# Performance work log

Hardware: AMD Instinct MI355X
Metric: run time of the kernel (lower is better)

## Reference

```python
import jax, jax.numpy as jnp
import numpy as np
from jax import lax

YXS = [(100, 250), (250, 250), (400, 250)]
HWS = [(50, 400), (50, 400), (50, 400)]
RATIO = 0.8
RCNN_THRES = 0.25
YOLO_THRES = 0.45
NMS_THRES = 0.4


def setup_inputs() -> dict:
    key = jax.random.key(0)
    ks = jax.random.split(key, 6)
    img = jax.random.uniform(ks[0], (1, 3, 500, 500), dtype=jnp.float32)
    patch0 = jax.random.normal(ks[1], (3, 50, 400), dtype=jnp.float32)
    patch1 = jax.random.normal(ks[2], (3, 50, 400), dtype=jnp.float32)
    patch2 = jax.random.normal(ks[3], (3, 50, 400), dtype=jnp.float32)
    rcnn_probs = jax.random.uniform(ks[4], (6144, 81), dtype=jnp.float32)
    boxes = jax.random.uniform(ks[5], (6144, 6), dtype=jnp.float32)
    return {"img": img, "patch0": patch0, "patch1": patch1, "patch2": patch2,
            "rcnn_probs": rcnn_probs, "boxes": boxes}


def _iou_matrix(b):
    # b: [M,4] center format (x, y, w, h) -> pairwise IoU [M,M]
    x1 = b[:, 0] - b[:, 2] * 0.5
    x2 = b[:, 0] + b[:, 2] * 0.5
    y1 = b[:, 1] - b[:, 3] * 0.5
    y2 = b[:, 1] + b[:, 3] * 0.5
    iw = jnp.maximum(jnp.minimum(x2[:, None], x2[None, :]) - jnp.maximum(x1[:, None], x1[None, :]), 0.0)
    ih = jnp.maximum(jnp.minimum(y2[:, None], y2[None, :]) - jnp.maximum(y1[:, None], y1[None, :]), 0.0)
    inter = iw * ih
    area = b[:, 2] * b[:, 3]
    union = area[:, None] + area[None, :] - inter
    return inter / jnp.maximum(union, 1e-12)


def _box_loss(c5, c4, mask):
    # per-box clamp/log loss on cls_conf (c5) and det_conf (c4), masked sum
    s = 1.0 / (0.5 - YOLO_THRES)
    l = (-jnp.clip((c5 - YOLO_THRES) * s, 0.0, 1.0) * jnp.log(1.0 - c5 + 0.01)
         - jnp.clip((c4 - YOLO_THRES) * s, 0.0, 1.0) * jnp.log(1.0 - c4 + 0.01))
    return jnp.sum(jnp.where(mask, l, 0.0))


def reference(img, patch0, patch1, patch2, rcnn_probs, boxes):
    # --- patch blending ---
    for (y, x), (h, w), p in zip(YXS, HWS, (patch0, patch1, patch2)):
        img = img.at[0, :, y - h // 2:y - h // 2 + h, x - w // 2:x - w // 2 + w].add(p)
    # clamp-violation penalty: (-img[img<0]).sum() + (img[img>1]-1).sum()
    p_loss = jnp.sum(jnp.maximum(-img, 0.0)) + jnp.sum(jnp.maximum(img - 1.0, 0.0))
    img = jnp.clip(img, 0.0, 1.0)

    # --- rcnn postprocessing loss ---
    prob = jnp.max(rcnn_probs[:, :-1], axis=-1)
    rmask = prob > RCNN_THRES
    b_prob = rcnn_probs[:, -1]
    r_loss = -jnp.sum(jnp.where(rmask, jnp.log(b_prob + 0.001), 0.0))
    r_loss += -jnp.sum(jnp.where(rmask,
                                 jnp.clip((prob - RCNN_THRES) / (0.3 - RCNN_THRES), 0.0, 1.0)
                                 * jnp.log(1.0 - prob + 0.001), 0.0))

    # --- yolo per-box loss + greedy IoU-NMS loss ---
    conf = boxes[:, 4]
    valid = conf > YOLO_THRES
    b_loss = _box_loss(boxes[:, 5], conf, valid)

    M = boxes.shape[0]
    order = jnp.argsort(-conf)
    sb = boxes[order]          # sorted by det_conf desc
    sv = valid[order]
    iou = _iou_matrix(sb[:, :4])  # [M,M]
    idx = jnp.arange(M)

    def body(keep, i):
        sup = (iou[i] > NMS_THRES) & (idx > i) & keep[i]
        return keep & ~sup, None

    keep, _ = lax.scan(body, sv, idx)
    b_nms_loss = _box_loss(sb[:, 5], sb[:, 4], keep)

    b_cnt = jnp.sum(valid.astype(jnp.float32))
    b_nms_cnt = jnp.maximum(jnp.sum(keep.astype(jnp.float32)), 1.0)
    yolo_loss = b_loss + b_nms_loss * (b_cnt / b_nms_cnt)

    loss = r_loss * RATIO + yolo_loss + p_loss
    return loss
```

## Files before the change

### kernel.cpp

```cpp
#include <hip/hip_runtime.h>
#include <hip/hip_bf16.h>
#include <stdint.h>

#define RCNN_THRES 0.25f
#define YOLO_THRES 0.45f
#define NMS_THRES  0.4f

#define M_BOXES 6144
#define NWORDS  96
#define SORT_N  4096

#define PL_BLOCKS 733
#define RL_BLOCKS 384
#define BL_BLOCKS 6
#define P_ELEMS  750000
#define MB_BLOCKS 1024

typedef unsigned long long u64;

__device__ inline float wave_sum(float v) {
#pragma unroll
    for (int o = 32; o > 0; o >>= 1) v += __shfl_xor(v, o);
    return v;
}
__device__ inline float wave_max(float v) {
#pragma unroll
    for (int o = 32; o > 0; o >>= 1) v = fmaxf(v, __shfl_xor(v, o));
    return v;
}

__device__ inline u64 readlane_u64(u64 v, int l) {
    unsigned lo = (unsigned)__builtin_amdgcn_readlane((int)(unsigned)v, l);
    unsigned hi = (unsigned)__builtin_amdgcn_readlane((int)(unsigned)(v >> 32), l);
    return ((u64)hi << 32) | (u64)lo;
}

__device__ inline float box_loss_term(float c5, float c4) {
    float a = fminf(fmaxf((c5 - YOLO_THRES) * 20.0f, 0.0f), 1.0f);
    float b = fminf(fmaxf((c4 - YOLO_THRES) * 20.0f, 0.0f), 1.0f);
    return -a * logf(1.0f - c5 + 0.01f) - b * logf(1.0f - c4 + 0.01f);
}

__device__ inline bool iou_gt(float x1a, float y1a, float x2a, float y2a, float aa,
                              float x1b, float y1b, float x2b, float y2b, float ab) {
    float iw = fmaxf(fminf(x2a, x2b) - fmaxf(x1a, x1b), 0.0f);
    float ih = fmaxf(fminf(y2a, y2b) - fmaxf(y1a, y1b), 0.0f);
    float inter = iw * ih;
    float uni = aa + ab - inter;
    return (inter / fmaxf(uni, 1e-12f)) > NMS_THRES;
}

__device__ inline u64 vw_word(int w, int nv) {
    int rem = nv - (w << 6);
    if (rem >= 64) return ~0ull;
    if (rem <= 0) return 0ull;
    return (1ull << rem) - 1ull;
}

__global__ __launch_bounds__(1024) void sort_and_losses(
    const float* __restrict__ boxes,
    const float* __restrict__ img, const float* __restrict__ p0,
    const float* __restrict__ p1, const float* __restrict__ p2,
    const float* __restrict__ probs,
    float* __restrict__ sx1, float* __restrict__ sy1,
    float* __restrict__ sx2, float* __restrict__ sy2,
    float* __restrict__ sarea, float* __restrict__ sconf, float* __restrict__ sc5,
    int* __restrict__ nvp, float* __restrict__ acc) {
    const int bid = blockIdx.x;
    const int tid = threadIdx.x, lane = tid & 63, wid = tid >> 6;

    if (bid == 0) {
        __shared__ u64 keys[SORT_N];
        __shared__ u64 bwords[96];
        __shared__ int wcnt[97];
#pragma unroll
        for (int s = 0; s < 6; ++s) {
            int p = tid + s * 1024;
            bool valid = boxes[p * 6 + 4] > YOLO_THRES;
            u64 b = __ballot(valid);
            int chunk = s * 16 + (tid >> 6);
            if (lane == 0) { bwords[chunk] = b; wcnt[chunk] = __popcll(b); }
        }
#pragma unroll
        for (int s = 0; s < 4; ++s) keys[tid + s * 1024] = 0ull;
        __syncthreads();
        if (tid == 0) {
            int run = 0;
            for (int i = 0; i < 96; ++i) { int t = wcnt[i]; wcnt[i] = run; run += t; }
            wcnt[96] = run;
            *nvp = run;
        }
        __syncthreads();
#pragma unroll
        for (int s = 0; s < 6; ++s) {
            int p = tid + s * 1024;
            if (boxes[p * 6 + 4] > YOLO_THRES) {
                int chunk = s * 16 + (tid >> 6);
                u64 b = bwords[chunk];
                int pos = wcnt[chunk] + __popcll(b & ((1ull << lane) - 1ull));
                if (pos < SORT_N) {
                    unsigned int bits = __float_as_uint(boxes[p * 6 + 4]);
                    keys[pos] = ((u64)bits << 13) | (u64)(8191 - p);
                }
            }
        }
        for (int k = 2; k <= SORT_N; k <<= 1) {
            for (int j = k >> 1; j > 0; j >>= 1) {
                __syncthreads();
#pragma unroll
                for (int s = 0; s < SORT_N / 2048; ++s) {
                    int q = tid + s * 1024;
                    int i = ((q & ~(j - 1)) << 1) | (q & (j - 1));
                    int p2 = i | j;
                    u64 a = keys[i], b = keys[p2];
                    bool up = ((i & k) == 0);
                    if ((a < b) == up) { keys[i] = b; keys[p2] = a; }
                }
            }
        }
        __syncthreads();
        const int nv = wcnt[96];
#pragma unroll
        for (int s = 0; s < 4; ++s) {
            int p = tid + s * 1024;
            if (p < nv) {
                int idx = 8191 - (int)(keys[p] & 0x1FFFull);
                const float* b6 = boxes + idx * 6;
                float x = b6[0], y = b6[1], wd = b6[2], ht = b6[3];
                sx1[p] = x - wd * 0.5f;
                sx2[p] = x + wd * 0.5f;
                sy1[p] = y - ht * 0.5f;
                sy2[p] = y + ht * 0.5f;
                sarea[p] = wd * ht;
                sconf[p] = b6[4];
                sc5[p] = b6[5];
            }
        }
        return;
    }

    __shared__ float fred[32];
    if (bid < 1 + PL_BLOCKS) {
        int e = (bid - 1) * 1024 + tid;
        float local = 0.0f;
        if (e < P_ELEMS) {
            float v = img[e];
            int c = e / 250000;
            int rem = e - c * 250000;
            int y = rem / 500;
            int x = rem - y * 500;
            if (x >= 50 && x < 450) {
                int px = x - 50;
                if (y >= 75 && y < 125)       v += p0[c * 20000 + (y - 75) * 400 + px];
                else if (y >= 225 && y < 275) v += p1[c * 20000 + (y - 225) * 400 + px];
                else if (y >= 375 && y < 425) v += p2[c * 20000 + (y - 375) * 400 + px];
            }
            local = fmaxf(-v, 0.0f) + fmaxf(v - 1.0f, 0.0f);
        }
        local = wave_sum(local);
        if (lane == 0) fred[wid] = local;
        __syncthreads();
        if (tid == 0) {
            float t = 0.0f;
#pragma unroll
            for (int k = 0; k < 16; ++k) t += fred[k];
            atomicAdd(&acc[0], t);
        }
    } else if (bid < 1 + PL_BLOCKS + RL_BLOCKS) {
        int row = (bid - 1 - PL_BLOCKS) * 16 + wid;
        const float* pr = probs + row * 81;
        float m = pr[lane];
        if (lane < 16) m = fmaxf(m, pr[64 + lane]);
        m = wave_max(m);
        float t = 0.0f;
        if (lane == 0 && m > RCNN_THRES) {
            float bp = pr[80];
            float cl = fminf(fmaxf((m - RCNN_THRES) * (1.0f / (0.3f - RCNN_THRES)), 0.0f), 1.0f);
            t = -logf(bp + 0.001f) - cl * logf(1.0f - m + 0.001f);
        }
        if (lane == 0) fred[wid] = t;
        __syncthreads();
        if (tid == 0) {
            float s = 0.0f;
#pragma unroll
            for (int k = 0; k < 16; ++k) s += fred[k];
            atomicAdd(&acc[1], s);
        }
    } else {
        int i = (bid - 1 - PL_BLOCKS - RL_BLOCKS) * 1024 + tid;
        float l = 0.0f, cnt = 0.0f;
        if (i < M_BOXES) {
            float conf = boxes[i * 6 + 4];
            if (conf > YOLO_THRES) {
                l = box_loss_term(boxes[i * 6 + 5], conf);
                cnt = 1.0f;
            }
        }
        l = wave_sum(l);
        cnt = wave_sum(cnt);
        if (lane == 0) { fred[wid] = l; fred[16 + wid] = cnt; }
        __syncthreads();
        if (tid == 0) {
            float tl = 0.0f, tc = 0.0f;
#pragma unroll
            for (int k = 0; k < 16; ++k) { tl += fred[k]; tc += fred[16 + k]; }
            atomicAdd(&acc[2], tl);
            atomicAdd(&acc[3], tc);
        }
    }
}

__global__ __launch_bounds__(256) void build_mask(
    const float* __restrict__ sx1, const float* __restrict__ sy1,
    const float* __restrict__ sx2, const float* __restrict__ sy2,
    const float* __restrict__ sarea, const int* __restrict__ nvp,
    u64* __restrict__ mask) {
    const int lane = threadIdx.x & 63, wid = threadIdx.x >> 6;
    const int nv = *nvp;
    int row = blockIdx.x * 4 + wid;
    if (row >= nv) return;
    const int nwa = (nv + 63) >> 6;
    float rx1 = sx1[row], ry1 = sy1[row], rx2 = sx2[row], ry2 = sy2[row];
    float ra = sarea[row];
    u64* mrow = mask + (size_t)row * NWORDS;
    for (int w = row >> 6; w < nwa; ++w) {
        int j = w * 64 + lane;
        bool pred = (j > row) && (j < nv) &&
                    iou_gt(rx1, ry1, rx2, ry2, ra,
                           sx1[j], sy1[j], sx2[j], sy2[j], sarea[j]);
        u64 bits = __ballot(pred);
        if (lane == 0) mrow[w] = bits;
    }
}

__global__ __launch_bounds__(512) void nms_walk(
    const float* __restrict__ acc, const int* __restrict__ nvp,
    const u64* __restrict__ mask,
    const float* __restrict__ sconf, const float* __restrict__ sc5,
    float* __restrict__ out) {
    __shared__ u64 SLICE[2][1024];
    __shared__ u64 SUPC[8][NWORDS];
    __shared__ u64 KW[NWORDS];
    __shared__ float fred[16];

    const int tid = threadIdx.x, lane = tid & 63, wid = tid >> 6;
    const int nv = *nvp;
    const int nwa = (nv + 63) >> 6;
    const int ngrp = (nwa + 3) >> 2;

    for (int i = tid; i < 8 * NWORDS; i += 512) ((u64*)SUPC)[i] = 0ull;
    for (int i = tid; i < NWORDS; i += 512) KW[i] = 0ull;
    {
        int r = tid >> 1, h = tid & 1;
        ulonglong2 m = *(const ulonglong2*)(mask + (size_t)r * NWORDS + 2 * h);
        *(ulonglong2*)&SLICE[0][r * 4 + 2 * h] = m;
    }
    __syncthreads();

    for (int g = 0; g < ngrp; ++g) {
        const int W = 4 * g;
        const int buf = g & 1;

        ulonglong2 stg{};
        const bool do_stage = (g + 1 < ngrp);
        if (do_stage) {
            int r = tid >> 1, h = tid & 1;
            stg = *(const ulonglong2*)(mask +
                    (size_t)((g + 1) * 256 + r) * NWORDS + (4 * (g + 1) + 2 * h));
        }

        if (wid == 0) {
            const u64* SL = SLICE[buf];
            ulonglong2 S0lo = *(const ulonglong2*)&SL[(0 * 64 + lane) * 4];
            ulonglong2 S0hi = *(const ulonglong2*)&SL[(0 * 64 + lane) * 4 + 2];
            ulonglong2 S1lo = *(const ulonglong2*)&SL[(1 * 64 + lane) * 4];
            ulonglong2 S1hi = *(const ulonglong2*)&SL[(1 * 64 + lane) * 4 + 2];
            ulonglong2 S2hi = *(const ulonglong2*)&SL[(2 * 64 + lane) * 4 + 2];
            ulonglong2 S3hi = *(const ulonglong2*)&SL[(3 * 64 + lane) * 4 + 2];
            (void)S1lo;

            u64 supW0 = 0ull, supW1 = 0ull, supW2 = 0ull, supW3 = 0ull;
#pragma unroll
            for (int k = 0; k < 8; ++k) {
                ulonglong2 a = *(const ulonglong2*)&SUPC[k][W];
                ulonglong2 b = *(const ulonglong2*)&SUPC[k][W + 2];
                supW0 |= a.x; supW1 |= a.y; supW2 |= b.x; supW3 |= b.y;
            }

            u64 gs1 = 0ull, gs2 = 0ull, gs3 = 0ull;
            u64 vw, cur, rem;
            vw = vw_word(W + 0, nv);
            if (vw) {
                cur = vw & ~supW0; rem = cur;
                while (rem) {
                    int t = __builtin_amdgcn_readfirstlane((int)__builtin_ctzll(rem));
                    u64 d = readlane_u64(S0lo.x, t);
                    gs1 |= readlane_u64(S0lo.y, t);
                    gs2 |= readlane_u64(S0hi.x, t);
                    gs3 |= readlane_u64(S0hi.y, t);
                    cur &= ~d; rem &= ~d; rem &= rem - 1;
                }
                if (lane == 0) KW[W + 0] = cur;
            }
            vw = vw_word(W + 1, nv);
            if (vw) {
                cur = vw & ~(supW1 | gs1); rem = cur;
                while (rem) {
                    int t = __builtin_amdgcn_readfirstlane((int)__builtin_ctzll(rem));
                    u64 d = readlane_u64(S1lo.y, t);
                    gs2 |= readlane_u64(S1hi.x, t);
                    gs3 |= readlane_u64(S1hi.y, t);
                    cur &= ~d; rem &= ~d; rem &= rem - 1;
                }
                if (lane == 0) KW[W + 1] = cur;
            }
            vw = vw_word(W + 2, nv);
            if (vw) {
                cur = vw & ~(supW2 | gs2); rem = cur;
                while (rem) {
                    int t = __builtin_amdgcn_readfirstlane((int)__builtin_ctzll(rem));
                    u64 d = readlane_u64(S2hi.x, t);
                    gs3 |= readlane_u64(S2hi.y, t);
                    cur &= ~d; rem &= ~d; rem &= rem - 1;
                }
                if (lane == 0) KW[W + 2] = cur;
            }
            vw = vw_word(W + 3, nv);
            if (vw) {
                cur = vw & ~(supW3 | gs3); rem = cur;
                while (rem) {
                    int t = __builtin_amdgcn_readfirstlane((int)__builtin_ctzll(rem));
                    u64 d = readlane_u64(S3hi.y, t);
                    cur &= ~d; rem &= ~d; rem &= rem - 1;
                }
                if (lane == 0) KW[W + 3] = cur;
            }
        }
        __syncthreads();

        if (do_stage) {
            int r = tid >> 1, h = tid & 1;
            *(ulonglong2*)&SLICE[buf ^ 1][r * 4 + 2 * h] = stg;
        }

        const int Wp4 = W + 4;
        const int nwrem = NWORDS - Wp4;
        if (nwrem > 0) {
            u64 kw0 = KW[W], kw1 = KW[W + 1], kw2 = KW[W + 2], kw3 = KW[W + 3];
            int idx = 0, nmine = 0;
            int b0 = 0, b1 = 0, b2 = 0, b3 = 0;
            const bool lactive = (2 * lane) < nwrem;
            const u64* bp = mask + Wp4 + 2 * lane;
            u64* scrow = &SUPC[wid][0];
#pragma unroll
            for (int c = 0; c < 4; ++c) {
                u64 k = (c == 0) ? kw0 : (c == 1) ? kw1 : (c == 2) ? kw2 : kw3;
                while (k) {
                    int bpos = (int)__builtin_ctzll(k); k &= k - 1;
                    if ((idx & 7) == wid) {
                        int row = ((W + c) << 6) + bpos;
                        int sl = nmine & 3;
                        if (sl == 0) b0 = row;
                        else if (sl == 1) b1 = row;
                        else if (sl == 2) b2 = row;
                        else b3 = row;
                        nmine++;
                        if ((nmine & 3) == 0 && lactive) {
                            ulonglong2 m0 = *(const ulonglong2*)(bp + (size_t)b0 * NWORDS);
                            ulonglong2 m1 = *(const ulonglong2*)(bp + (size_t)b1 * NWORDS);
                            ulonglong2 m2 = *(const ulonglong2*)(bp + (size_t)b2 * NWORDS);
                            ulonglong2 m3 = *(const ulonglong2*)(bp + (size_t)b3 * NWORDS);
                            scrow[Wp4 + 2 * lane]     |= m0.x | m1.x | m2.x | m3.x;
                            scrow[Wp4 + 2 * lane + 1] |= m0.y | m1.y | m2.y | m3.y;
                        }
                    }
                    idx++;
                }
            }
            if ((nmine & 3) != 0 && lactive) {
                int n = nmine & 3;
                int a1 = (n > 1) ? b1 : b0, a2 = (n > 2) ? b2 : b0;
                ulonglong2 m0 = *(const ulonglong2*)(bp + (size_t)b0 * NWORDS);
                ulonglong2 m1 = *(const ulonglong2*)(bp + (size_t)a1 * NWORDS);
                ulonglong2 m2 = *(const ulonglong2*)(bp + (size_t)a2 * NWORDS);
                scrow[Wp4 + 2 * lane]     |= m0.x | m1.x | m2.x;
                scrow[Wp4 + 2 * lane + 1] |= m0.y | m1.y | m2.y;
            }
        }
        __syncthreads();
    }

    float nl = 0.0f, nc = 0.0f;
    for (int p = tid; p < M_BOXES; p += 512) {
        if ((KW[p >> 6] >> (p & 63)) & 1ull) {
            nl += box_loss_term(sc5[p], sconf[p]);
            nc += 1.0f;
        }
    }
    nl = wave_sum(nl);
    nc = wave_sum(nc);
    if (lane == 0) { fred[wid] = nl; fred[8 + wid] = nc; }
    __syncthreads();
    if (tid == 0) {
        float tnl = 0.0f, tnc = 0.0f;
#pragma unroll
        for (int k = 0; k < 8; ++k) { tnl += fred[k]; tnc += fred[8 + k]; }
        float p_loss = acc[0], r_loss = acc[1], b_loss = acc[2], b_cnt = acc[3];
        float yolo = b_loss + tnl * (b_cnt / fmaxf(tnc, 1.0f));
        out[0] = r_loss * 0.8f + yolo + p_loss;
    }
}

extern "C" void kernel_launch(void* const* d_in, const int* in_sizes, int n_in,
                              void* d_out, int out_size, void* d_ws, size_t ws_size,
                              hipStream_t stream) {
    const float* img   = (const float*)d_in[0];
    const float* p0    = (const float*)d_in[1];
    const float* p1    = (const float*)d_in[2];
    const float* p2    = (const float*)d_in[3];
    const float* probs = (const float*)d_in[4];
    const float* boxes = (const float*)d_in[5];
    float* out = (float*)d_out;

    char* ws = (char*)d_ws;
    float* acc = (float*)ws;
    int* nvp = (int*)(ws + 32);
    float* sx1 = (float*)(ws + 1024);
    float* sy1 = sx1 + M_BOXES;
    float* sx2 = sy1 + M_BOXES;
    float* sy2 = sx2 + M_BOXES;
    float* sarea = sy2 + M_BOXES;
    float* sconf = sarea + M_BOXES;
    float* sc5 = sconf + M_BOXES;
    u64* mask = (u64*)(ws + 173056);

    hipMemsetAsync(acc, 0, 64, stream);
    sort_and_losses<<<1 + PL_BLOCKS + RL_BLOCKS + BL_BLOCKS, 1024, 0, stream>>>(
        boxes, img, p0, p1, p2, probs,
        sx1, sy1, sx2, sy2, sarea, sconf, sc5, nvp, acc);
    build_mask<<<MB_BLOCKS, 256, 0, stream>>>(sx1, sy1, sx2, sy2, sarea, nvp, mask);
    nms_walk<<<1, 512, 0, stream>>>(acc, nvp, mask, sconf, sc5, out);
}
```

Measured before the change: 176.3 us.

## Replace single-block bitonic sort with multi-block rank-counting sort

Swaps the single-workgroup compaction plus bitonic sort of valid boxes for a rank sort spread over 96 blocks. Each block loads every key into shared memory, and each box's rank comes from counting the larger keys with 16 lanes per box. The sorted box fields are then scattered to their rank positions. This removes a long serial critical path on one CU but makes every ranking block do O(N) loads and comparisons, which is O(N^2) work in total.

```diff
diff --git a/kernel.cpp b/kernel.cpp
--- a/kernel.cpp
+++ b/kernel.cpp
@@ -10,6 +10,7 @@
 #define NWORDS  96
 #define SORT_N  4096
 
+#define RK_BLOCKS 96
 #define PL_BLOCKS 733
 #define RL_BLOCKS 384
 #define BL_BLOCKS 6
@@ -69,79 +70,61 @@
     const int bid = blockIdx.x;
     const int tid = threadIdx.x, lane = tid & 63, wid = tid >> 6;
 
-    if (bid == 0) {
-        __shared__ u64 keys[SORT_N];
-        __shared__ u64 bwords[96];
-        __shared__ int wcnt[97];
+    if (bid < RK_BLOCKS) {
+        __shared__ u64 KL[M_BOXES];
+        __shared__ float cred[16];
+        float myvalid = 0.0f;
 #pragma unroll
         for (int s = 0; s < 6; ++s) {
             int p = tid + s * 1024;
-            bool valid = boxes[p * 6 + 4] > YOLO_THRES;
-            u64 b = __ballot(valid);
-            int chunk = s * 16 + (tid >> 6);
-            if (lane == 0) { bwords[chunk] = b; wcnt[chunk] = __popcll(b); }
-        }
-#pragma unroll
-        for (int s = 0; s < 4; ++s) keys[tid + s * 1024] = 0ull;
-        __syncthreads();
-        if (tid == 0) {
-            int run = 0;
-            for (int i = 0; i < 96; ++i) { int t = wcnt[i]; wcnt[i] = run; run += t; }
-            wcnt[96] = run;
-            *nvp = run;
-        }
-        __syncthreads();
-#pragma unroll
-        for (int s = 0; s < 6; ++s) {
-            int p = tid + s * 1024;
-            if (boxes[p * 6 + 4] > YOLO_THRES) {
-                int chunk = s * 16 + (tid >> 6);
-                u64 b = bwords[chunk];
-                int pos = wcnt[chunk] + __popcll(b & ((1ull << lane) - 1ull));
-                if (pos < SORT_N) {
-                    unsigned int bits = __float_as_uint(boxes[p * 6 + 4]);
-                    keys[pos] = ((u64)bits << 13) | (u64)(8191 - p);
-                }
-            }
-        }
-        for (int k = 2; k <= SORT_N; k <<= 1) {
-            for (int j = k >> 1; j > 0; j >>= 1) {
-                __syncthreads();
-#pragma unroll
-                for (int s = 0; s < SORT_N / 2048; ++s) {
-                    int q = tid + s * 1024;
-                    int i = ((q & ~(j - 1)) << 1) | (q & (j - 1));
-                    int p2 = i | j;
-                    u64 a = keys[i], b = keys[p2];
-                    bool up = ((i & k) == 0);
-                    if ((a < b) == up) { keys[i] = b; keys[p2] = a; }
-                }
-            }
-        }
-        __syncthreads();
-        const int nv = wcnt[96];
-#pragma unroll
-        for (int s = 0; s < 4; ++s) {
-            int p = tid + s * 1024;
-            if (p < nv) {
-                int idx = 8191 - (int)(keys[p] & 0x1FFFull);
-                const float* b6 = boxes + idx * 6;
+            float conf = boxes[p * 6 + 4];
+            u64 key = 0ull;
+            if (conf > YOLO_THRES) {
+                key = ((u64)__float_as_uint(conf) << 13) | (u64)(8191 - p);
+                myvalid += 1.0f;
+            }
+            KL[p] = key;
+        }
+        __syncthreads();
+        if (bid == 0) {
+            float c = wave_sum(myvalid);
+            if (lane == 0) cred[wid] = c;
+            __syncthreads();
+            if (tid == 0) {
+                float t = 0.0f;
+#pragma unroll
+                for (int k = 0; k < 16; ++k) t += cred[k];
+                *nvp = (int)(t + 0.5f);
+            }
+        }
+        const int box = bid * 64 + (tid >> 4);
+        const int seg = tid & 15;
+        const u64 mykey = KL[box];
+        int cnt = 0;
+        for (int i = seg; i < M_BOXES; i += 16)
+            cnt += (KL[i] > mykey) ? 1 : 0;
+#pragma unroll
+        for (int o = 1; o < 16; o <<= 1) cnt += __shfl_xor(cnt, o);
+        if (seg == 0 && mykey != 0ull) {
+            int rank = cnt;
+            if (rank < SORT_N) {
+                const float* b6 = boxes + box * 6;
                 float x = b6[0], y = b6[1], wd = b6[2], ht = b6[3];
-                sx1[p] = x - wd * 0.5f;
-                sx2[p] = x + wd * 0.5f;
-                sy1[p] = y - ht * 0.5f;
-                sy2[p] = y + ht * 0.5f;
-                sarea[p] = wd * ht;
-                sconf[p] = b6[4];
-                sc5[p] = b6[5];
+                sx1[rank] = x - wd * 0.5f;
+                sx2[rank] = x + wd * 0.5f;
+                sy1[rank] = y - ht * 0.5f;
+                sy2[rank] = y + ht * 0.5f;
+                sarea[rank] = wd * ht;
+                sconf[rank] = b6[4];
+                sc5[rank] = b6[5];
             }
         }
         return;
     }
 
     __shared__ float fred[32];
-    if (bid < 1 + PL_BLOCKS) {
-        int e = (bid - 1) * 1024 + tid;
+    if (bid < RK_BLOCKS + PL_BLOCKS) {
+        int e = (bid - RK_BLOCKS) * 1024 + tid;
         float local = 0.0f;
         if (e < P_ELEMS) {
             float v = img[e];
@@ -166,8 +149,8 @@
             for (int k = 0; k < 16; ++k) t += fred[k];
             atomicAdd(&acc[0], t);
         }
-    } else if (bid < 1 + PL_BLOCKS + RL_BLOCKS) {
-        int row = (bid - 1 - PL_BLOCKS) * 16 + wid;
+    } else if (bid < RK_BLOCKS + PL_BLOCKS + RL_BLOCKS) {
+        int row = (bid - RK_BLOCKS - PL_BLOCKS) * 16 + wid;
         const float* pr = probs + row * 81;
         float m = pr[lane];
         if (lane < 16) m = fmaxf(m, pr[64 + lane]);
@@ -187,7 +170,7 @@
             atomicAdd(&acc[1], s);
         }
     } else {
-        int i = (bid - 1 - PL_BLOCKS - RL_BLOCKS) * 1024 + tid;
+        int i = (bid - RK_BLOCKS - PL_BLOCKS - RL_BLOCKS) * 1024 + tid;
         float l = 0.0f, cnt = 0.0f;
         if (i < M_BOXES) {
             float conf = boxes[i * 6 + 4];
@@ -435,7 +418,7 @@
     u64* mask = (u64*)(ws + 173056);
 
     hipMemsetAsync(acc, 0, 64, stream);
-    sort_and_losses<<<1 + PL_BLOCKS + RL_BLOCKS + BL_BLOCKS, 1024, 0, stream>>>(
+    sort_and_losses<<<RK_BLOCKS + PL_BLOCKS + RL_BLOCKS + BL_BLOCKS, 1024, 0, stream>>>(
         boxes, img, p0, p1, p2, probs,
         sx1, sy1, sx2, sy2, sarea, sconf, sc5, nvp, acc);
     build_mask<<<MB_BLOCKS, 256, 0, stream>>>(sx1, sy1, sx2, sy2, sarea, nvp, mask);
```

After: 157.9 us. 10.4% less time.
